# Performance work log

Measured on AMD Instinct MI355X. Metric: run time of the kernel, lower is better.

The kernel has to match this reference:

```python
import jax, jax.numpy as jnp
import numpy as np


def _grid_sample_paste(m, boxes, img_h, img_w):
    """Bilinear, align_corners=False, zero padding; separable because the
    affine grid is an outer product of per-row and per-col coordinates.
    m: [N, Hm, Wm] float, boxes: [N, 4] xyxy in output-image coords.
    Returns [N, img_h, img_w]."""
    N, Hm, Wm = m.shape
    x0, y0, x1, y1 = boxes[:, 0:1], boxes[:, 1:2], boxes[:, 2:3], boxes[:, 3:4]
    ys = jnp.arange(img_h, dtype=m.dtype) + 0.5  # pixel centers
    xs = jnp.arange(img_w, dtype=m.dtype) + 0.5
    gy = (ys[None, :] - y0) / (y1 - y0) * 2 - 1  # [N, img_h] in [-1,1]
    gx = (xs[None, :] - x0) / (x1 - x0) * 2 - 1  # [N, img_w]
    # align_corners=False: pixel coord = (g+1)*size/2 - 0.5
    py = (gy + 1) * (Hm * 0.5) - 0.5
    px = (gx + 1) * (Wm * 0.5) - 0.5

    def interp(vals, p, axis, size):
        f = jnp.floor(p)
        i0 = f.astype(jnp.int32)
        w1 = (p - f).astype(vals.dtype)
        w0 = 1.0 - w1

        def gather(idx):
            valid = ((idx >= 0) & (idx < size)).astype(vals.dtype)
            idxc = jnp.clip(idx, 0, size - 1)
            if axis == 2:
                g = jnp.take_along_axis(vals, idxc[:, None, :], axis=2)
                return g * valid[:, None, :]
            else:
                g = jnp.take_along_axis(vals, idxc[:, :, None], axis=1)
                return g * valid[:, :, None]

        if axis == 2:
            return gather(i0) * w0[:, None, :] + gather(i0 + 1) * w1[:, None, :]
        else:
            return gather(i0) * w0[:, :, None] + gather(i0 + 1) * w1[:, :, None]

    mx = interp(m, px, axis=2, size=Wm)   # [N, Hm, img_w]
    return interp(mx, py, axis=1, size=Hm)  # [N, img_h, img_w]


def setup_inputs() -> dict:
    key = jax.random.key(0)
    k1, k2, k3, k4, k5 = jax.random.split(key, 5)
    N, Hm, Wm = 128, 28, 28
    in_h, in_w = 736, 1184
    img_h, img_w = 800, 1280
    masks = jax.random.uniform(k1, (N, 1, Hm, Wm), dtype=jnp.float32)
    # valid xyxy boxes in detector-input coordinates
    bx0 = jax.random.uniform(k2, (N,), minval=0.0, maxval=in_w - 64.0)
    by0 = jax.random.uniform(k3, (N,), minval=0.0, maxval=in_h - 64.0)
    bw = 16.0 + jax.random.uniform(k4, (N,), maxval=256.0)
    bh = 16.0 + jax.random.uniform(k5, (N,), maxval=256.0)
    boxes = jnp.stack([bx0, by0,
                       jnp.minimum(bx0 + bw, in_w * 1.0),
                       jnp.minimum(by0 + bh, in_h * 1.0)], axis=1).astype(jnp.float32)
    return {"masks": masks, "boxes": boxes, "img_h": img_h, "img_w": img_w,
            "in_h": in_h, "in_w": in_w}


def reference(masks, boxes, img_h, img_w, in_h, in_w):
    # my_detector_postprocess: scale boxes to output resolution, clip to image
    sx = img_w / in_w
    sy = img_h / in_h
    scale = jnp.array([sx, sy, sx, sy], dtype=boxes.dtype)
    b = boxes * scale
    b = jnp.stack([jnp.clip(b[:, 0], 0.0, img_w), jnp.clip(b[:, 1], 0.0, img_h),
                   jnp.clip(b[:, 2], 0.0, img_w), jnp.clip(b[:, 3], 0.0, img_h)], axis=1)
    # my_paste_masks_in_image (GPU path, skip_empty=False), soft masks returned
    return _grid_sample_paste(masks[:, 0], b, img_h, img_w)
```

## Files before the change

kernel.cpp:

```cpp
#include <hip/hip_runtime.h>
#include <math.h>

#define TPB 256

__device__ __forceinline__ float bilin(const float* __restrict__ mb,
                                       float px, float vy0, float vy1,
                                       int ry0, int ry1, int Hm, int Wm) {
    float fx = floorf(px);
    int ix = (int)fx;
    float wx1 = px - fx;
    float wx0 = 1.f - wx1;
    float vx0 = (ix >= 0 && ix < Wm) ? wx0 : 0.f;
    float vx1 = (ix + 1 >= 0 && ix + 1 < Wm) ? wx1 : 0.f;
    int rx0 = min(max(ix, 0), Wm - 1);
    int rx1 = min(max(ix + 1, 0), Wm - 1);
    float top = mb[ry0 * Wm + rx0] * vx0 + mb[ry0 * Wm + rx1] * vx1;
    float bot = mb[ry1 * Wm + rx0] * vx0 + mb[ry1 * Wm + rx1] * vx1;
    return top * vy0 + bot * vy1;
}

__device__ __forceinline__ float sample_one(const float* __restrict__ mb,
                                            float px, float py, int Hm, int Wm) {
    if (py <= -1.f || py >= (float)Hm || px <= -1.f || px >= (float)Wm) return 0.f;
    float fy = floorf(py);
    int iy = (int)fy;
    float wy1 = py - fy, wy0 = 1.f - wy1;
    float vy0 = (iy >= 0 && iy < Hm) ? wy0 : 0.f;
    float vy1 = (iy + 1 >= 0 && iy + 1 < Hm) ? wy1 : 0.f;
    int ry0 = min(max(iy, 0), Hm - 1);
    int ry1 = min(max(iy + 1, 0), Hm - 1);
    return bilin(mb, px, vy0, vy1, ry0, ry1, Hm, Wm);
}

__global__ void paste(const float* __restrict__ masks,
                      const float* __restrict__ boxes,
                      const int* __restrict__ p_img_h,
                      const int* __restrict__ p_img_w,
                      const int* __restrict__ p_in_h,
                      const int* __restrict__ p_in_w,
                      float* __restrict__ out,
                      int HW, int Hm, int Wm) {
    __shared__ float4 sP;
    const int n = blockIdx.z;
    const int img_w = p_img_w[0];

    if (threadIdx.x == 0) {
        float fw = (float)img_w, fh = (float)p_img_h[0];
        float sx = fw / (float)p_in_w[0];
        float sy = fh / (float)p_in_h[0];
        float x0 = fminf(fmaxf(boxes[4*n+0] * sx, 0.f), fw);
        float y0 = fminf(fmaxf(boxes[4*n+1] * sy, 0.f), fh);
        float x1 = fminf(fmaxf(boxes[4*n+2] * sx, 0.f), fw);
        float y1 = fminf(fmaxf(boxes[4*n+3] * sy, 0.f), fh);
        sP = make_float4(x0, y0, (float)Wm / (x1 - x0), (float)Hm / (y1 - y0));
    }
    __syncthreads();
    const float4 P = sP;

    int q = blockIdx.x * blockDim.x + threadIdx.x;
    int base = q * 4;
    if (base >= HW) return;
    int y = base / img_w;
    int x = base - y * img_w;
    float* optr = out + (size_t)n * HW + base;
    const float* mb = masks + (size_t)n * Hm * Wm;

    bool aligned = (((size_t)optr & 15) == 0);
    if (aligned && (x + 3 < img_w) && (base + 3 < HW)) {
        float py = ((float)y + 0.5f - P.y) * P.w - 0.5f;
        float px0 = ((float)x + 0.5f - P.x) * P.z - 0.5f;
        float px3 = px0 + 3.f * P.z;
        if (py <= -1.f || py >= (float)Hm || px3 <= -1.f || px0 >= (float)Wm) {
            *(float4*)optr = make_float4(0.f, 0.f, 0.f, 0.f);
        } else {
            float fy = floorf(py);
            int iy = (int)fy;
            float wy1 = py - fy, wy0 = 1.f - wy1;
            float vy0 = (iy >= 0 && iy < Hm) ? wy0 : 0.f;
            float vy1 = (iy + 1 >= 0 && iy + 1 < Hm) ? wy1 : 0.f;
            int ry0 = min(max(iy, 0), Hm - 1);
            int ry1 = min(max(iy + 1, 0), Hm - 1);
            float4 r;
            r.x = bilin(mb, px0, vy0, vy1, ry0, ry1, Hm, Wm);
            r.y = bilin(mb, px0 + P.z, vy0, vy1, ry0, ry1, Hm, Wm);
            r.z = bilin(mb, px0 + 2.f * P.z, vy0, vy1, ry0, ry1, Hm, Wm);
            r.w = bilin(mb, px3, vy0, vy1, ry0, ry1, Hm, Wm);
            *(float4*)optr = r;
        }
    } else {
        int yy = y, xx = x;
        for (int i = 0; i < 4; ++i) {
            if (base + i >= HW) break;
            float py = ((float)yy + 0.5f - P.y) * P.w - 0.5f;
            float px = ((float)xx + 0.5f - P.x) * P.z - 0.5f;
            optr[i] = sample_one(mb, px, py, Hm, Wm);
            xx++;
            if (xx >= img_w) { xx = 0; yy++; }
        }
    }
}

extern "C" void kernel_launch(void* const* d_in, const int* in_sizes, int n_in,
                              void* d_out, int out_size, void* d_ws, size_t ws_size,
                              hipStream_t stream) {
    const float* masks  = (const float*)d_in[0];
    const float* boxes  = (const float*)d_in[1];
    const int* p_img_h  = (const int*)d_in[2];
    const int* p_img_w  = (const int*)d_in[3];
    const int* p_in_h   = (const int*)d_in[4];
    const int* p_in_w   = (const int*)d_in[5];

    int N = in_sizes[1] / 4;
    int mask_hw = in_sizes[0] / N;
    int Wm = (int)(sqrtf((float)mask_hw) + 0.5f);
    int Hm = mask_hw / Wm;
    int HW = out_size / N;

    int nquad = (HW + 3) / 4;
    dim3 grid((nquad + TPB - 1) / TPB, 1, N);
    hipLaunchKernelGGL(paste, grid, dim3(TPB), 0, stream,
                       masks, boxes, p_img_h, p_img_w, p_in_h, p_in_w,
                       (float*)d_out, HW, Hm, Wm);
}
```

Baseline: 534.9 us.

## Split paste into bulk zero-fill kernel and per-box bounding-region sampling kernel

Replaces the single per-pixel kernel with two launches. The first is a grid-stride float4 kernel that zero-fills the whole output. The second samples only the pixels inside each box's footprint, with one block column per mask and rows strided over grid.y. This removes the bounds and branch work the old kernel ran for every background pixel, and focuses the sampling on the small box regions. The cost is a second kernel launch and scalar (non-vectorised) stores inside the boxes. Those regions are written again after the zero fill, so they take two writes.

```diff
diff --git a/kernel.cpp b/kernel.cpp
--- a/kernel.cpp
+++ b/kernel.cpp
@@ -1,11 +1,20 @@
 #include <hip/hip_runtime.h>
 #include <math.h>
 
-#define TPB 256
+__global__ __launch_bounds__(256) void zero_out(float4* __restrict__ out4, int nf4,
+                                                float* __restrict__ out, int out_size) {
+    int gid = blockIdx.x * blockDim.x + threadIdx.x;
+    int stride = gridDim.x * blockDim.x;
+    const float4 z = make_float4(0.f, 0.f, 0.f, 0.f);
+    for (int i = gid; i < nf4; i += stride) out4[i] = z;
+    if (gid == 0) {
+        for (int k = nf4 * 4; k < out_size; ++k) out[k] = 0.f;
+    }
+}
 
-__device__ __forceinline__ float bilin(const float* __restrict__ mb,
-                                       float px, float vy0, float vy1,
-                                       int ry0, int ry1, int Hm, int Wm) {
+__device__ __forceinline__ float bilin(const float* __restrict__ r0,
+                                       const float* __restrict__ r1,
+                                       float px, float vy0, float vy1, int Wm) {
     float fx = floorf(px);
     int ix = (int)fx;
     float wx1 = px - fx;
@@ -14,88 +23,54 @@
     float vx1 = (ix + 1 >= 0 && ix + 1 < Wm) ? wx1 : 0.f;
     int rx0 = min(max(ix, 0), Wm - 1);
     int rx1 = min(max(ix + 1, 0), Wm - 1);
-    float top = mb[ry0 * Wm + rx0] * vx0 + mb[ry0 * Wm + rx1] * vx1;
-    float bot = mb[ry1 * Wm + rx0] * vx0 + mb[ry1 * Wm + rx1] * vx1;
+    float top = r0[rx0] * vx0 + r0[rx1] * vx1;
+    float bot = r1[rx0] * vx0 + r1[rx1] * vx1;
     return top * vy0 + bot * vy1;
 }
 
-__device__ __forceinline__ float sample_one(const float* __restrict__ mb,
-                                            float px, float py, int Hm, int Wm) {
-    if (py <= -1.f || py >= (float)Hm || px <= -1.f || px >= (float)Wm) return 0.f;
-    float fy = floorf(py);
-    int iy = (int)fy;
-    float wy1 = py - fy, wy0 = 1.f - wy1;
-    float vy0 = (iy >= 0 && iy < Hm) ? wy0 : 0.f;
-    float vy1 = (iy + 1 >= 0 && iy + 1 < Hm) ? wy1 : 0.f;
-    int ry0 = min(max(iy, 0), Hm - 1);
-    int ry1 = min(max(iy + 1, 0), Hm - 1);
-    return bilin(mb, px, vy0, vy1, ry0, ry1, Hm, Wm);
-}
+__global__ __launch_bounds__(128) void paint_box(const float* __restrict__ masks,
+                       const float* __restrict__ boxes,
+                       const int* __restrict__ p_img_h,
+                       const int* __restrict__ p_img_w,
+                       const int* __restrict__ p_in_h,
+                       const int* __restrict__ p_in_w,
+                       float* __restrict__ out,
+                       int HW, int Hm, int Wm) {
+    const int n = blockIdx.x;
+    const int img_w = p_img_w[0];
+    const int img_h = HW / img_w;
 
-__global__ void paste(const float* __restrict__ masks,
-                      const float* __restrict__ boxes,
-                      const int* __restrict__ p_img_h,
-                      const int* __restrict__ p_img_w,
-                      const int* __restrict__ p_in_h,
-                      const int* __restrict__ p_in_w,
-                      float* __restrict__ out,
-                      int HW, int Hm, int Wm) {
-    __shared__ float4 sP;
-    const int n = blockIdx.z;
-    const int img_w = p_img_w[0];
+    float fw = (float)img_w, fh = (float)img_h;
+    float sx = fw / (float)p_in_w[0];
+    float sy = fh / (float)p_in_h[0];
+    float x0 = fminf(fmaxf(boxes[4*n+0] * sx, 0.f), fw);
+    float y0 = fminf(fmaxf(boxes[4*n+1] * sy, 0.f), fh);
+    float x1 = fminf(fmaxf(boxes[4*n+2] * sx, 0.f), fw);
+    float y1 = fminf(fmaxf(boxes[4*n+3] * sy, 0.f), fh);
+    float swx = (float)Wm / (x1 - x0);
+    float swy = (float)Hm / (y1 - y0);
 
-    if (threadIdx.x == 0) {
-        float fw = (float)img_w, fh = (float)p_img_h[0];
-        float sx = fw / (float)p_in_w[0];
-        float sy = fh / (float)p_in_h[0];
-        float x0 = fminf(fmaxf(boxes[4*n+0] * sx, 0.f), fw);
-        float y0 = fminf(fmaxf(boxes[4*n+1] * sy, 0.f), fh);
-        float x1 = fminf(fmaxf(boxes[4*n+2] * sx, 0.f), fw);
-        float y1 = fminf(fmaxf(boxes[4*n+3] * sy, 0.f), fh);
-        sP = make_float4(x0, y0, (float)Wm / (x1 - x0), (float)Hm / (y1 - y0));
-    }
-    __syncthreads();
-    const float4 P = sP;
+    int xlo = max(0,     (int)floorf(x0 - 0.5f / swx - 0.5f) - 1);
+    int xhi = min(img_w, (int)ceilf (x0 + ((float)Wm + 0.5f) / swx - 0.5f) + 2);
+    int ylo = max(0,     (int)floorf(y0 - 0.5f / swy - 0.5f) - 1);
+    int yhi = min(img_h, (int)ceilf (y0 + ((float)Hm + 0.5f) / swy - 0.5f) + 2);
 
-    int q = blockIdx.x * blockDim.x + threadIdx.x;
-    int base = q * 4;
-    if (base >= HW) return;
-    int y = base / img_w;
-    int x = base - y * img_w;
-    float* optr = out + (size_t)n * HW + base;
     const float* mb = masks + (size_t)n * Hm * Wm;
+    float* ob = out + (size_t)n * HW;
 
-    bool aligned = (((size_t)optr & 15) == 0);
-    if (aligned && (x + 3 < img_w) && (base + 3 < HW)) {
-        float py = ((float)y + 0.5f - P.y) * P.w - 0.5f;
-        float px0 = ((float)x + 0.5f - P.x) * P.z - 0.5f;
-        float px3 = px0 + 3.f * P.z;
-        if (py <= -1.f || py >= (float)Hm || px3 <= -1.f || px0 >= (float)Wm) {
-            *(float4*)optr = make_float4(0.f, 0.f, 0.f, 0.f);
-        } else {
-            float fy = floorf(py);
-            int iy = (int)fy;
-            float wy1 = py - fy, wy0 = 1.f - wy1;
-            float vy0 = (iy >= 0 && iy < Hm) ? wy0 : 0.f;
-            float vy1 = (iy + 1 >= 0 && iy + 1 < Hm) ? wy1 : 0.f;
-            int ry0 = min(max(iy, 0), Hm - 1);
-            int ry1 = min(max(iy + 1, 0), Hm - 1);
-            float4 r;
-            r.x = bilin(mb, px0, vy0, vy1, ry0, ry1, Hm, Wm);
-            r.y = bilin(mb, px0 + P.z, vy0, vy1, ry0, ry1, Hm, Wm);
-            r.z = bilin(mb, px0 + 2.f * P.z, vy0, vy1, ry0, ry1, Hm, Wm);
-            r.w = bilin(mb, px3, vy0, vy1, ry0, ry1, Hm, Wm);
-            *(float4*)optr = r;
-        }
-    } else {
-        int yy = y, xx = x;
-        for (int i = 0; i < 4; ++i) {
-            if (base + i >= HW) break;
-            float py = ((float)yy + 0.5f - P.y) * P.w - 0.5f;
-            float px = ((float)xx + 0.5f - P.x) * P.z - 0.5f;
-            optr[i] = sample_one(mb, px, py, Hm, Wm);
-            xx++;
-            if (xx >= img_w) { xx = 0; yy++; }
+    for (int y = ylo + blockIdx.y; y < yhi; y += gridDim.y) {
+        float py = ((float)y + 0.5f - y0) * swy - 0.5f;
+        float fy = floorf(py);
+        int iy = (int)fy;
+        float wy1 = py - fy, wy0 = 1.f - wy1;
+        float vy0 = (iy >= 0 && iy < Hm) ? wy0 : 0.f;
+        float vy1 = (iy + 1 >= 0 && iy + 1 < Hm) ? wy1 : 0.f;
+        const float* r0 = mb + (size_t)min(max(iy, 0), Hm - 1) * Wm;
+        const float* r1 = mb + (size_t)min(max(iy + 1, 0), Hm - 1) * Wm;
+        float* orow = ob + (size_t)y * img_w;
+        for (int x = xlo + (int)threadIdx.x; x < xhi; x += (int)blockDim.x) {
+            float px = ((float)x + 0.5f - x0) * swx - 0.5f;
+            orow[x] = bilin(r0, r1, px, vy0, vy1, Wm);
         }
     }
 }
@@ -116,9 +91,12 @@
     int Hm = mask_hw / Wm;
     int HW = out_size / N;
 
-    int nquad = (HW + 3) / 4;
-    dim3 grid((nquad + TPB - 1) / TPB, 1, N);
-    hipLaunchKernelGGL(paste, grid, dim3(TPB), 0, stream,
+    int nf4 = out_size / 4;
+    int zblocks = 4096;
+    hipLaunchKernelGGL(zero_out, dim3(zblocks), dim3(256), 0, stream,
+                       (float4*)d_out, nf4, (float*)d_out, out_size);
+
+    hipLaunchKernelGGL(paint_box, dim3(N, 512), dim3(128), 0, stream,
                        masks, boxes, p_img_h, p_img_w, p_in_h, p_in_w,
                        (float*)d_out, HW, Hm, Wm);
 }
```

Measured after the change: 553.9 us. 3.6% more time.
